# Kernel optimization log

Hardware: AMD Instinct MI355X
Metric: run time of the kernel (lower is better)

The kernel has to match this reference:

```python
import jax, jax.numpy as jnp
import numpy as np

N_SAMPLES = 4_000_000
N_BINS = 100
VMIN, VMAX = -5.0, 5.0


def setup_inputs() -> dict:
    key = jax.random.key(0)
    k1, k2, k3 = jax.random.split(key, 3)
    eps = jax.random.normal(k1, (N_SAMPLES, 1), dtype=jnp.float32)
    # learned params, initialized as in the torch module
    p = jax.random.normal(k2, (N_BINS + 1,), dtype=jnp.float32) / 5.0
    b = jax.random.normal(k3, (1,), dtype=jnp.float32) + VMIN
    points = jnp.linspace(VMIN, VMAX, N_BINS, dtype=jnp.float32).reshape(1, N_BINS)
    return {"eps": eps, "p": p, "b": b, "points": points}


def _to_positive(x):
    return jnp.exp(x) + 0.001


def reference(eps, p, b, points):
    n = points.shape[1]
    int_length = (VMAX - VMIN) / (n - 1)
    # delta_h is detached in the original (torch .detach())
    delta_h = int_length * jax.lax.stop_gradient(_to_positive(p[1:n]))  # [n-1]
    # sequential cumsum loop in torch == prefix sum; delta_bias[0] = b
    prefix = jnp.concatenate([jnp.zeros((1,), delta_h.dtype), jnp.cumsum(delta_h)])  # [n]
    delta_bias = b[0] + prefix  # [n]; grad flows only through b
    # brute-force bucketize: count breakpoints <= eps
    index = jnp.sum((eps - points) >= 0, axis=1)  # [N], values in 0..n
    start_idx = jnp.maximum(index - 1, 0)  # [N]
    db = delta_bias[start_idx]  # [N]
    start_pts = jax.lax.stop_gradient(points[0][start_idx])  # [N]
    k = _to_positive(p[index])  # [N]
    delta_x = eps - start_pts[:, None]  # [N,1]
    return delta_x * k[:, None] + db[:, None]  # [N,1]
```

## Files before the change

kernel.cpp:

```cpp
#include <hip/hip_runtime.h>

#define NBINS 100
#define PWL_VMIN -5.0f
#define PWL_VMAX 5.0f

__global__ __launch_bounds__(128) void build_tables_kernel(
    const float* __restrict__ p,
    const float* __restrict__ b,
    float* __restrict__ ws)
{
    __shared__ float s_k[NBINS + 1];
    const int t = threadIdx.x;
    if (t <= NBINS) {
        float k = expf(p[t]) + 0.001f;
        s_k[t] = k;
        ws[t]  = k;
    }
    __syncthreads();
    if (t == 0) {
        const float int_length = (PWL_VMAX - PWL_VMIN) / (float)(NBINS - 1);
        const float b0 = b[0];
        float acc = 0.0f;
        ws[NBINS + 1 + 0] = b0;
        for (int i = 1; i < NBINS; ++i) {
            acc += int_length * s_k[i];
            ws[NBINS + 1 + i] = b0 + acc;
        }
    }
}

__global__ __launch_bounds__(256) void pwl_kernel(
    const float* __restrict__ eps,
    const float* __restrict__ points,
    const float* __restrict__ ws,
    float* __restrict__ out,
    int n4)
{
    __shared__ float s_pts[NBINS];
    __shared__ float s_k[NBINS + 1];
    __shared__ float s_db[NBINS];

    const int t = threadIdx.x;
    if (t < NBINS) {
        s_pts[t] = points[t];
        s_db[t]  = ws[NBINS + 1 + t];
    }
    if (t <= NBINS) s_k[t] = ws[t];
    __syncthreads();

    const float inv_step = (float)(NBINS - 1) / (PWL_VMAX - PWL_VMIN);

    const float4* __restrict__ in4  = reinterpret_cast<const float4*>(eps);
    float4* __restrict__       out4 = reinterpret_cast<float4*>(out);

    for (int i = blockIdx.x * blockDim.x + t; i < n4; i += gridDim.x * blockDim.x) {
        float4 e4 = in4[i];
        float ev[4] = {e4.x, e4.y, e4.z, e4.w};
        float r[4];
#pragma unroll
        for (int j = 0; j < 4; ++j) {
            const float e = ev[j];
            int idx = (int)floorf((e - PWL_VMIN) * inv_step) + 1;
            idx = max(0, min(idx, NBINS));
            while (idx < NBINS && s_pts[idx] <= e) ++idx;
            while (idx > 0 && s_pts[idx - 1] > e) --idx;
            const int si = max(idx - 1, 0);
            r[j] = (e - s_pts[si]) * s_k[idx] + s_db[si];
        }
        float4 o4;
        o4.x = r[0]; o4.y = r[1]; o4.z = r[2]; o4.w = r[3];
        out4[i] = o4;
    }
}

extern "C" void kernel_launch(void* const* d_in, const int* in_sizes, int n_in,
                              void* d_out, int out_size, void* d_ws, size_t ws_size,
                              hipStream_t stream)
{
    const float* eps    = (const float*)d_in[0];
    const float* p      = (const float*)d_in[1];
    const float* b      = (const float*)d_in[2];
    const float* points = (const float*)d_in[3];
    float* out          = (float*)d_out;
    float* ws           = (float*)d_ws;

    build_tables_kernel<<<1, 128, 0, stream>>>(p, b, ws);

    const int n  = out_size;
    const int n4 = n / 4;
    const int block = 256;
    int grid = (n4 + block - 1) / block;
    if (grid > 2048) grid = 2048;
    pwl_kernel<<<grid, block, 0, stream>>>(eps, points, ws, out, n4);

    const int tail = n & 3;
    if (tail) {
    }
}
```

Before: 76.50 us.

## Fuse table build into main kernel and prefetch first eps loads before setup

Removes the separate single-block table-building kernel, so each block computes exp(p) and the prefix sum in shared memory itself. The first two float4 loads of eps are issued before the table setup to hide its latency. This saves one kernel launch and a global workspace round trip. In exchange, every block redoes the serial 100-step prefix sum on one thread.

Measured after the change: 77.96 us. About the same (+1.9%).

```diff
diff --git a/kernel.cpp b/kernel.cpp
--- a/kernel.cpp
+++ b/kernel.cpp
@@ -4,35 +4,11 @@
 #define PWL_VMIN -5.0f
 #define PWL_VMAX 5.0f
 
-__global__ __launch_bounds__(128) void build_tables_kernel(
+__global__ __launch_bounds__(256) void pwl_fused_kernel(
+    const float* __restrict__ eps,
     const float* __restrict__ p,
     const float* __restrict__ b,
-    float* __restrict__ ws)
-{
-    __shared__ float s_k[NBINS + 1];
-    const int t = threadIdx.x;
-    if (t <= NBINS) {
-        float k = expf(p[t]) + 0.001f;
-        s_k[t] = k;
-        ws[t]  = k;
-    }
-    __syncthreads();
-    if (t == 0) {
-        const float int_length = (PWL_VMAX - PWL_VMIN) / (float)(NBINS - 1);
-        const float b0 = b[0];
-        float acc = 0.0f;
-        ws[NBINS + 1 + 0] = b0;
-        for (int i = 1; i < NBINS; ++i) {
-            acc += int_length * s_k[i];
-            ws[NBINS + 1 + i] = b0 + acc;
-        }
-    }
-}
-
-__global__ __launch_bounds__(256) void pwl_kernel(
-    const float* __restrict__ eps,
     const float* __restrict__ points,
-    const float* __restrict__ ws,
     float* __restrict__ out,
     int n4)
 {
@@ -40,21 +16,39 @@
     __shared__ float s_k[NBINS + 1];
     __shared__ float s_db[NBINS];
 
-    const int t = threadIdx.x;
-    if (t < NBINS) {
-        s_pts[t] = points[t];
-        s_db[t]  = ws[NBINS + 1 + t];
+    const int t      = threadIdx.x;
+    const int tid    = blockIdx.x * blockDim.x + t;
+    const int stride = gridDim.x * blockDim.x;
+
+    const float4* __restrict__ in4  = reinterpret_cast<const float4*>(eps);
+    float4* __restrict__       out4 = reinterpret_cast<float4*>(out);
+
+    const int i0 = tid;
+    const int i1 = tid + stride;
+    float4 e0, e1;
+    const bool h0 = (i0 < n4);
+    const bool h1 = (i1 < n4);
+    if (h0) e0 = in4[i0];
+    if (h1) e1 = in4[i1];
+
+    if (t < NBINS)  s_pts[t] = points[t];
+    if (t <= NBINS) s_k[t]   = expf(p[t]) + 0.001f;
+    __syncthreads();
+    if (t == 0) {
+        const float int_length = (PWL_VMAX - PWL_VMIN) / (float)(NBINS - 1);
+        const float b0 = b[0];
+        float acc = 0.0f;
+        s_db[0] = b0;
+        for (int i = 1; i < NBINS; ++i) {
+            acc += int_length * s_k[i];
+            s_db[i] = b0 + acc;
+        }
     }
-    if (t <= NBINS) s_k[t] = ws[t];
     __syncthreads();
 
     const float inv_step = (float)(NBINS - 1) / (PWL_VMAX - PWL_VMIN);
 
-    const float4* __restrict__ in4  = reinterpret_cast<const float4*>(eps);
-    float4* __restrict__       out4 = reinterpret_cast<float4*>(out);
-
-    for (int i = blockIdx.x * blockDim.x + t; i < n4; i += gridDim.x * blockDim.x) {
-        float4 e4 = in4[i];
+    auto process = [&](float4 e4) -> float4 {
         float ev[4] = {e4.x, e4.y, e4.z, e4.w};
         float r[4];
 #pragma unroll
@@ -67,9 +61,14 @@
             const int si = max(idx - 1, 0);
             r[j] = (e - s_pts[si]) * s_k[idx] + s_db[si];
         }
-        float4 o4;
-        o4.x = r[0]; o4.y = r[1]; o4.z = r[2]; o4.w = r[3];
-        out4[i] = o4;
+        return make_float4(r[0], r[1], r[2], r[3]);
+    };
+
+    if (h0) out4[i0] = process(e0);
+    if (h1) out4[i1] = process(e1);
+
+    for (int i = tid + 2 * stride; i < n4; i += stride) {
+        out4[i] = process(in4[i]);
     }
 }
 
@@ -82,18 +81,10 @@
     const float* b      = (const float*)d_in[2];
     const float* points = (const float*)d_in[3];
     float* out          = (float*)d_out;
-    float* ws           = (float*)d_ws;
-
-    build_tables_kernel<<<1, 128, 0, stream>>>(p, b, ws);
 
     const int n  = out_size;
     const int n4 = n / 4;
     const int block = 256;
-    int grid = (n4 + block - 1) / block;
-    if (grid > 2048) grid = 2048;
-    pwl_kernel<<<grid, block, 0, stream>>>(eps, points, ws, out, n4);
-
-    const int tail = n & 3;
-    if (tail) {
-    }
+    int grid = 2048;
+    pwl_fused_kernel<<<grid, block, 0, stream>>>(eps, p, b, points, out, n4);
 }
```
